# Kernel optimization log

Hardware: AMD Instinct MI355X
Metric: run time of the kernel (lower is better)

The kernel has to match this reference:

```python
import jax, jax.numpy as jnp
import numpy as np

W_SZ = 128  # window size
H = 8       # heads
DH = 64     # dim per head


def _ln(x, w, b):
    mu = x.mean(-1, keepdims=True)
    var = ((x - mu) ** 2).mean(-1, keepdims=True)
    return (x - mu) / jnp.sqrt(var + 1e-5) * w + b


def _rot_half(x):
    x1, x2 = jnp.split(x, 2, axis=-1)
    return jnp.concatenate([-x2, x1], axis=-1)


def _split_heads(t):  # [b, n, h*d] -> [b*h, n, d]
    b, n, hd = t.shape
    return t.reshape(b, n, H, hd // H).transpose(0, 2, 1, 3).reshape(b * H, n, hd // H)


def _merge_heads(t):  # [b*h, n, d] -> [b, n, h*d]
    bh, n, d = t.shape
    return t.reshape(bh // H, H, n, d).transpose(0, 2, 1, 3).reshape(bh // H, n, H * d)


def _poolformer(tokens, tok_emb, gpos_emb, g_norm_w, g_norm_b, g_Wq, g_Wkv, g_Wo, g_bo,
                gff_norm_w, gff_norm_b, gff_W1, gff_b1, gff_W2, gff_b2,
                la_norm_w, la_norm_b, la_Wq, la_Wkv, la_Wo, la_bo,
                lff_norm_w, lff_norm_b, lff_W1, lff_b1, lff_W2, lff_b2,
                out_norm_w, out_norm_b, out_W, out_b):
    b, n = tokens.shape
    nw = n // W_SZ  # n is a multiple of W_SZ, so no padding branch is taken
    x = tok_emb[tokens]                       # [b, n, D]
    D = x.shape[-1]
    g = x.reshape(b, nw, W_SZ, D).mean(axis=2) + gpos_emb[:nw][None]  # [b, nw, D]
    # inline rotary freqs over dim_head (SinusoidalEmbeddings)
    inv_freq = 1.0 / (10000.0 ** (jnp.arange(0, DH, 2, dtype=jnp.float32) / DH))
    fr = jnp.arange(n, dtype=jnp.float32)[:, None] * inv_freq[None, :]
    freqs = jnp.concatenate([fr, fr], axis=-1)  # [n, DH]
    cos_f, sin_f = jnp.cos(freqs), jnp.sin(freqs)
    scale = DH ** -0.5
    # causal masks (True = masked out)
    lmask = jnp.arange(2 * W_SZ)[None, :] > (jnp.arange(W_SZ)[:, None] + W_SZ)  # [W, 2W]
    gmask = jnp.arange(nw - 1)[None, :] >= jnp.arange(nw)[:, None]              # [nw, nw-1]
    full_mask = jnp.concatenate([
        jnp.broadcast_to(gmask[:, None, :], (nw, W_SZ, nw - 1)),
        jnp.broadcast_to(lmask[None], (nw, W_SZ, 2 * W_SZ)),
    ], axis=-1)[None]
    depth = la_Wq.shape[0]
    for l in range(depth):
        # --- global-token transformer (weights shared across layers) ---
        gn = _ln(g, g_norm_w, g_norm_b).reshape(b * nw, 1, D)
        ctx = jnp.concatenate([gn, x.reshape(b * nw, W_SZ, D)], axis=1)  # with_self=True
        q = _split_heads(gn @ g_Wq)
        k, v = jnp.split(ctx @ g_Wkv, 2, axis=-1)
        k = _split_heads(k); v = _split_heads(v)
        # causal mask is vacuous here (i=1, j=1+W -> triu diag beyond matrix)
        attn = jax.nn.softmax(jnp.einsum('bid,bjd->bij', q, k) * (k.shape[-1] ** -0.5), axis=-1)
        go = _merge_heads(jnp.einsum('bij,bjd->bid', attn, v)) @ g_Wo + g_bo
        g = g + go.reshape(b, nw, D)
        gn = _ln(g, gff_norm_w, gff_norm_b)
        g = g + (jax.nn.gelu(gn @ gff_W1 + gff_b1, approximate=False) @ gff_W2 + gff_b2)
        # --- local windowed attention with global tokens ---
        xn = _ln(x, la_norm_w[l], la_norm_b[l])
        q = _split_heads(xn @ la_Wq[l])
        k, v = jnp.split(xn @ la_Wkv[l], 2, axis=-1)
        k = _split_heads(k)
        q = q * cos_f + _rot_half(q) * sin_f
        k = k * cos_f + _rot_half(k) * sin_f
        qw = q.reshape(b * H, nw, W_SZ, DH)
        kpad = jnp.pad(k.reshape(b * H, nw, W_SZ, DH), ((0, 0), (1, 0), (0, 0), (0, 0)))
        kcat = jnp.concatenate([kpad[:, :-1], kpad[:, 1:]], axis=2)  # [bH, nw, 2W, DH]
        vcat = kcat  # faithful to source closure bug: v is overwritten with windowed k
        gk, gv = jnp.split(g[:, :-1] @ la_Wkv[l], 2, axis=-1)  # global tokens -> kv (un-normed)
        gk = _split_heads(gk); gv = _split_heads(gv)           # [bH, nw-1, DH]
        kf = jnp.concatenate([jnp.broadcast_to(gk[:, None], (b * H, nw, nw - 1, DH)), kcat], axis=2)
        vf = jnp.concatenate([jnp.broadcast_to(gv[:, None], (b * H, nw, nw - 1, DH)), vcat], axis=2)
        sim = jnp.einsum('bwid,bwjd->bwij', qw, kf) * scale
        sim = jnp.where(full_mask, -jnp.finfo(sim.dtype).max, sim)
        ao = jnp.einsum('bwij,bwjd->bwid', jax.nn.softmax(sim, axis=-1), vf)
        x = x + _merge_heads(ao.reshape(b * H, n, DH)) @ la_Wo[l] + la_bo[l]
        xn = _ln(x, lff_norm_w[l], lff_norm_b[l])
        x = x + (jax.nn.gelu(xn @ lff_W1[l] + lff_b1[l], approximate=False) @ lff_W2[l] + lff_b2[l])
    return _ln(x, out_norm_w, out_norm_b) @ out_W + out_b


def setup_inputs() -> dict:
    key = jax.random.key(0)
    ks = jax.random.split(key, 16)
    B, N, D, V, DEPTH, FF = 1, 2048, 512, 32000, 2, 2048
    INNER = H * DH
    s = 0.02
    rn = lambda k, shape: jax.random.normal(k, shape, dtype=jnp.float32) * s
    inp = {}
    inp['tokens'] = jax.random.randint(ks[0], (B, N), 0, V, dtype=jnp.int32)
    inp['tok_emb'] = rn(ks[1], (V, D))
    inp['gpos_emb'] = rn(ks[2], (N // W_SZ, D))
    inp['g_norm_w'] = jnp.ones((D,)); inp['g_norm_b'] = jnp.zeros((D,))
    inp['g_Wq'] = rn(ks[3], (D, INNER)); inp['g_Wkv'] = rn(ks[4], (D, 2 * INNER))
    inp['g_Wo'] = rn(ks[5], (INNER, D)); inp['g_bo'] = jnp.zeros((D,))
    inp['gff_norm_w'] = jnp.ones((D,)); inp['gff_norm_b'] = jnp.zeros((D,))
    inp['gff_W1'] = rn(ks[6], (D, FF)); inp['gff_b1'] = jnp.zeros((FF,))
    inp['gff_W2'] = rn(ks[7], (FF, D)); inp['gff_b2'] = jnp.zeros((D,))
    inp['la_norm_w'] = jnp.ones((DEPTH, D)); inp['la_norm_b'] = jnp.zeros((DEPTH, D))
    inp['la_Wq'] = rn(ks[8], (DEPTH, D, INNER)); inp['la_Wkv'] = rn(ks[9], (DEPTH, D, 2 * INNER))
    inp['la_Wo'] = rn(ks[10], (DEPTH, INNER, D)); inp['la_bo'] = jnp.zeros((DEPTH, D))
    inp['lff_norm_w'] = jnp.ones((DEPTH, D)); inp['lff_norm_b'] = jnp.zeros((DEPTH, D))
    inp['lff_W1'] = rn(ks[11], (DEPTH, D, FF)); inp['lff_b1'] = jnp.zeros((DEPTH, FF))
    inp['lff_W2'] = rn(ks[12], (DEPTH, FF, D)); inp['lff_b2'] = jnp.zeros((DEPTH, D))
    inp['out_norm_w'] = jnp.ones((D,)); inp['out_norm_b'] = jnp.zeros((D,))
    inp['out_W'] = rn(ks[13], (D, V)); inp['out_b'] = jnp.zeros((V,))
    return inp


def reference(tokens, tok_emb, gpos_emb, g_norm_w, g_norm_b, g_Wq, g_Wkv, g_Wo, g_bo,
              gff_norm_w, gff_norm_b, gff_W1, gff_b1, gff_W2, gff_b2,
              la_norm_w, la_norm_b, la_Wq, la_Wkv, la_Wo, la_bo,
              lff_norm_w, lff_norm_b, lff_W1, lff_b1, lff_W2, lff_b2,
              out_norm_w, out_norm_b, out_W, out_b):
    return _poolformer(tokens, tok_emb, gpos_emb, g_norm_w, g_norm_b, g_Wq, g_Wkv, g_Wo, g_bo,
                       gff_norm_w, gff_norm_b, gff_W1, gff_b1, gff_W2, gff_b2,
                       la_norm_w, la_norm_b, la_Wq, la_Wkv, la_Wo, la_bo,
                       lff_norm_w, lff_norm_b, lff_W1, lff_b1, lff_W2, lff_b2,
                       out_norm_w, out_norm_b, out_W, out_b)
```

## Files before the change

kernel.cpp:

```cpp
#include <hip/hip_runtime.h>
#include <math.h>

#define N_TOK 2048
#define DM    512
#define NW    16
#define WSZ   128
#define NH    8
#define DHD   64
#define FFD   2048
#define VOC   32000
#define NDEPTH 2

typedef unsigned short u16;
typedef unsigned int   u32;
typedef __attribute__((ext_vector_type(8))) short bf16x8;
typedef __attribute__((ext_vector_type(4))) float f32x4;

__device__ __forceinline__ float gelu_f(float v){
  return 0.5f*v*(1.0f+erff(v*0.70710678118654752440f));
}
__device__ __forceinline__ u16 f2bf(float f){
  u32 u = __float_as_uint(f);
  u += 0x7fffu + ((u >> 16) & 1u);
  return (u16)(u >> 16);
}

__global__ void k_embed(const int* __restrict__ tok, const float* __restrict__ emb,
                        float* __restrict__ x, u16* __restrict__ xb){
  int idx = blockIdx.x*256 + threadIdx.x;
  int i = idx >> 9, d = idx & 511;
  float v = emb[(size_t)tok[i]*DM + d];
  x[idx] = v;
  xb[idx] = f2bf(v);
}

__global__ void k_pool(const float* __restrict__ x, const float* __restrict__ gpos,
                       float* __restrict__ g){
  int idx = blockIdx.x*256 + threadIdx.x;
  int w = idx >> 9, d = idx & 511;
  const float* p = x + (size_t)(w*WSZ)*DM + d;
  float s = 0.f;
  #pragma unroll 8
  for (int i=0;i<WSZ;i++) s += p[(size_t)i*DM];
  g[idx] = s*(1.f/WSZ) + gpos[idx];
}

__global__ void k_rotab(float* __restrict__ ct, float* __restrict__ st){
  int idx = blockIdx.x*256 + threadIdx.x;
  int i = idx >> 5, j = idx & 31;
  double inv = pow(10000.0, -(double)j/32.0);
  double a = (double)i*inv;
  ct[idx] = (float)cos(a);
  st[idx] = (float)sin(a);
}

__global__ void k_rope(float* __restrict__ q, float* __restrict__ k,
                       const float* __restrict__ ct, const float* __restrict__ st){
  int idx = blockIdx.x*256 + threadIdx.x;
  int i = idx >> 8;
  int h = (idx >> 5) & 7;
  int j = idx & 31;
  float c = ct[i*32+j], s = st[i*32+j];
  size_t base = (size_t)i*DM + h*DHD + j;
  float q0=q[base], q1=q[base+32];
  q[base]    = q0*c - q1*s;
  q[base+32] = q1*c + q0*s;
  float k0=k[base], k1=k[base+32];
  k[base]    = k0*c - k1*s;
  k[base+32] = k1*c + k0*s;
}

template<bool BF>
__global__ __launch_bounds__(256) void k_ln(const float* __restrict__ in,
                     float* __restrict__ outf, u16* __restrict__ outb,
                     const float* __restrict__ w, const float* __restrict__ b){
  int r = blockIdx.x;
  const float2* p2 = reinterpret_cast<const float2*>(in + (size_t)r*DM);
  float2 v = p2[threadIdx.x];
  float s = v.x+v.y, ss = v.x*v.x + v.y*v.y;
  #pragma unroll
  for (int o=32;o;o>>=1){ s += __shfl_xor(s,o); ss += __shfl_xor(ss,o); }
  __shared__ float sm[4], sm2[4];
  int wv = threadIdx.x >> 6;
  if ((threadIdx.x & 63) == 0){ sm[wv]=s; sm2[wv]=ss; }
  __syncthreads();
  if (threadIdx.x == 0){
    float t=sm[0]+sm[1]+sm[2]+sm[3], t2=sm2[0]+sm2[1]+sm2[2]+sm2[3];
    float mu = t*(1.f/DM);
    float var = t2*(1.f/DM) - mu*mu;
    sm[0]=mu; sm2[0]=rsqrtf(var + 1e-5f);
  }
  __syncthreads();
  float mu = sm[0], rs = sm2[0];
  float2 wv2 = reinterpret_cast<const float2*>(w)[threadIdx.x];
  float2 bv2 = reinterpret_cast<const float2*>(b)[threadIdx.x];
  float ox = (v.x-mu)*rs*wv2.x + bv2.x;
  float oy = (v.y-mu)*rs*wv2.y + bv2.y;
  if (BF){
    reinterpret_cast<u32*>(outb)[(size_t)r*256 + threadIdx.x] =
        (u32)f2bf(ox) | ((u32)f2bf(oy) << 16);
  } else {
    float2 o; o.x = ox; o.y = oy;
    reinterpret_cast<float2*>(outf + (size_t)r*DM)[threadIdx.x] = o;
  }
}

__global__ __launch_bounds__(256) void k_wcvt(const float* __restrict__ in, int ldn, int c0,
                        u16* __restrict__ out, int K){
  __shared__ float t[32][33];
  const int tx = threadIdx.x & 31, ty = threadIdx.x >> 5;
  const int n0 = blockIdx.x*32, k0 = blockIdx.y*32;
  #pragma unroll
  for (int r = ty; r < 32; r += 8)
    t[r][tx] = in[(size_t)(k0+r)*ldn + c0 + n0 + tx];
  __syncthreads();
  #pragma unroll
  for (int r = ty; r < 32; r += 8)
    out[(size_t)(n0+r)*K + k0 + tx] = f2bf(t[tx][r]);
}

template<bool BIAS,bool RES,bool GELU,bool SBF,bool SF32>
__global__ __launch_bounds__(256) void k_mgemm(
    const u16* __restrict__ A, int lda,
    const u16* __restrict__ Bt,
    float* __restrict__ C, int ldc,
    u16* __restrict__ Cb, int ldcb,
    const float* __restrict__ bias, int K)
{
  __shared__ __align__(16) u16 As[128*40];
  __shared__ __align__(16) u16 Bs[128*40];
  const int tid = threadIdx.x;
  const int bm0 = blockIdx.y*128, bn0 = blockIdx.x*128;
  const int lane = tid & 63, wid = tid >> 6;
  const int wr = wid >> 1, wc = wid & 1;
  const int r16 = lane & 15, ko = lane >> 4;
  const int srow = tid >> 1, koff = (tid & 1) * 16;
  const u16* Ap = A + (size_t)(bm0 + srow)*lda + koff;
  const u16* Bp = Bt + (size_t)(bn0 + srow)*K + koff;
  const u32 lwa = (u32)srow*40 + (u32)koff;

  f32x4 acc[4][4];
  #pragma unroll
  for (int m=0;m<4;m++)
    #pragma unroll
    for (int n=0;n<4;n++)
      acc[m][n] = (f32x4){0.f,0.f,0.f,0.f};

  for (int kk = 0; kk < K; kk += 32){
    const uint4 a0 = *reinterpret_cast<const uint4*>(Ap + kk);
    const uint4 a1 = *reinterpret_cast<const uint4*>(Ap + kk + 8);
    const uint4 b0 = *reinterpret_cast<const uint4*>(Bp + kk);
    const uint4 b1 = *reinterpret_cast<const uint4*>(Bp + kk + 8);
    *reinterpret_cast<uint4*>(&As[lwa])     = a0;
    *reinterpret_cast<uint4*>(&As[lwa + 8]) = a1;
    *reinterpret_cast<uint4*>(&Bs[lwa])     = b0;
    *reinterpret_cast<uint4*>(&Bs[lwa + 8]) = b1;
    __syncthreads();
    bf16x8 af[4], bfr[4];
    #pragma unroll
    for (int m=0;m<4;m++)
      af[m] = *reinterpret_cast<const bf16x8*>(&As[(u32)(wr*64 + m*16 + r16)*40 + (u32)ko*8]);
    #pragma unroll
    for (int n=0;n<4;n++)
      bfr[n] = *reinterpret_cast<const bf16x8*>(&Bs[(u32)(wc*64 + n*16 + r16)*40 + (u32)ko*8]);
    #pragma unroll
    for (int m=0;m<4;m++)
      #pragma unroll
      for (int n=0;n<4;n++)
        acc[m][n] = __builtin_amdgcn_mfma_f32_16x16x32_bf16(af[m], bfr[n], acc[m][n], 0, 0, 0);
    __syncthreads();
  }

  const int crow0 = bm0 + wr*64, ccol0 = bn0 + wc*64;
  #pragma unroll
  for (int m=0;m<4;m++){
    #pragma unroll
    for (int j=0;j<4;j++){
      const int row = crow0 + m*16 + ko*4 + j;
      #pragma unroll
      for (int n=0;n<4;n++){
        const int col = ccol0 + n*16 + r16;
        float v = acc[m][n][j];
        if (BIAS) v += bias[col];
        if (GELU) v = gelu_f(v);
        if (RES)  v += C[(size_t)row*ldc + col];
        if (SF32) C[(size_t)row*ldc + col] = v;
        if (SBF)  Cb[(size_t)row*ldcb + col] = f2bf(v);
      }
    }
  }
}

__global__ __launch_bounds__(256) void k_psum(
    const float* __restrict__ A, int lda,
    const float* __restrict__ B, int ldb,
    float* __restrict__ P, int N, int M)
{
  __shared__ __align__(16) float As[16][68];
  const int tid = threadIdx.x;
  const int cg = tid & 63, rg = tid >> 6;
  const int n0 = blockIdx.x*256 + cg*4;
  const int k0 = blockIdx.y*64;
  for (int e = tid; e < 16*64; e += 256){
    int r = e >> 6, c = e & 63;
    As[r][c] = (r < M) ? A[(size_t)r*lda + k0 + c] : 0.f;
  }
  __syncthreads();
  float4 acc0 = {0.f,0.f,0.f,0.f}, acc1 = acc0, acc2 = acc0, acc3 = acc0;
  const float* Bp = B + (size_t)k0*ldb + n0;
  #pragma unroll 4
  for (int k4 = 0; k4 < 64; k4 += 4){
    float a0[4], a1[4], a2[4], a3[4];
    *reinterpret_cast<float4*>(a0) = *reinterpret_cast<const float4*>(&As[rg*4+0][k4]);
    *reinterpret_cast<float4*>(a1) = *reinterpret_cast<const float4*>(&As[rg*4+1][k4]);
    *reinterpret_cast<float4*>(a2) = *reinterpret_cast<const float4*>(&As[rg*4+2][k4]);
    *reinterpret_cast<float4*>(a3) = *reinterpret_cast<const float4*>(&As[rg*4+3][k4]);
    #pragma unroll
    for (int j = 0; j < 4; j++){
      const float4 bv = *reinterpret_cast<const float4*>(Bp + (size_t)(k4+j)*ldb);
      acc0.x = fmaf(a0[j], bv.x, acc0.x); acc0.y = fmaf(a0[j], bv.y, acc0.y);
      acc0.z = fmaf(a0[j], bv.z, acc0.z); acc0.w = fmaf(a0[j], bv.w, acc0.w);
      acc1.x = fmaf(a1[j], bv.x, acc1.x); acc1.y = fmaf(a1[j], bv.y, acc1.y);
      acc1.z = fmaf(a1[j], bv.z, acc1.z); acc1.w = fmaf(a1[j], bv.w, acc1.w);
      acc2.x = fmaf(a2[j], bv.x, acc2.x); acc2.y = fmaf(a2[j], bv.y, acc2.y);
      acc2.z = fmaf(a2[j], bv.z, acc2.z); acc2.w = fmaf(a2[j], bv.w, acc2.w);
      acc3.x = fmaf(a3[j], bv.x, acc3.x); acc3.y = fmaf(a3[j], bv.y, acc3.y);
      acc3.z = fmaf(a3[j], bv.z, acc3.z); acc3.w = fmaf(a3[j], bv.w, acc3.w);
    }
  }
  float* Pp = P + ((size_t)blockIdx.y*16 + rg*4)*N + n0;
  *reinterpret_cast<float4*>(Pp)       = acc0;
  *reinterpret_cast<float4*>(Pp + N)   = acc1;
  *reinterpret_cast<float4*>(Pp + 2*N) = acc2;
  *reinterpret_cast<float4*>(Pp + 3*N) = acc3;
}

template<bool BIAS,bool RES,bool GELU>
__global__ __launch_bounds__(256) void k_red(
    const float* __restrict__ P, int N, int S, int M,
    float* __restrict__ C, int ldc, const float* __restrict__ bias)
{
  int idx = blockIdx.x*256 + threadIdx.x;
  int r = idx / N, n = idx - r*N;
  if (r >= M) return;
  float v = 0.f;
  for (int s = 0; s < S; s++) v += P[((size_t)s*16 + r)*N + n];
  if (BIAS) v += bias[n];
  if (GELU) v = gelu_f(v);
  if (RES)  v += C[(size_t)r*ldc + n];
  C[(size_t)r*ldc + n] = v;
}

__global__ __launch_bounds__(64) void k_gattn(
    const float* __restrict__ gq, const float* __restrict__ kvg,
    const float* __restrict__ kvx, float* __restrict__ out)
{
  const int w = blockIdx.x >> 3, h = blockIdx.x & 7;
  const int lane = threadIdx.x;
  __shared__ float qs[64];
  __shared__ float p[129];
  qs[lane] = gq[(size_t)w*DM + h*DHD + lane];
  __syncthreads();
  for (int c=0;c<3;c++){
    int j = c*64 + lane;
    if (j < 129){
      const float* kp = (j==0) ? &kvg[(size_t)w*1024 + h*DHD]
                               : &kvx[(size_t)(w*WSZ + j-1)*1024 + h*DHD];
      float s = 0.f;
      for (int d=0;d<64;d++) s = fmaf(qs[d], kp[d], s);
      p[j] = s*0.125f;
    }
  }
  __syncthreads();
  float mx = -3.4e38f;
  for (int j=lane;j<129;j+=64) mx = fmaxf(mx, p[j]);
  #pragma unroll
  for (int o=32;o;o>>=1) mx = fmaxf(mx, __shfl_xor(mx,o));
  float sum = 0.f;
  for (int j=lane;j<129;j+=64){ float e = expf(p[j]-mx); p[j]=e; sum+=e; }
  #pragma unroll
  for (int o=32;o;o>>=1) sum += __shfl_xor(sum,o);
  const float rs = 1.f/sum;
  __syncthreads();
  float o_ = 0.f;
  for (int j=0;j<129;j++){
    const float* vp = (j==0) ? &kvg[(size_t)w*1024 + 512 + h*DHD]
                             : &kvx[(size_t)(w*WSZ + j-1)*1024 + 512 + h*DHD];
    o_ = fmaf(p[j], vp[lane], o_);
  }
  out[(size_t)w*DM + h*DHD + lane] = o_*rs;
}

__global__ __launch_bounds__(256) void k_lattn_m(
    const float* __restrict__ q, const float* __restrict__ k,
    const float* __restrict__ gkv, u16* __restrict__ ob)
{
  __shared__ __align__(16) u16 smem[43136];
  __shared__ float rsum[64];
  u16* Ks = smem;
  u16* Qs = smem + 19584;
  u16* Vt = smem + 24192;
  u16* Ps = smem;
  const int bid = blockIdx.x;
  const int half = bid & 1, h = (bid >> 1) & 7, w = bid >> 4;
  const int tid = threadIdx.x;
  const int lane = tid & 63, wv = tid >> 6;
  const int c16 = lane & 15, ko = lane >> 4;
  const int q0 = w*WSZ + half*64;
  #pragma unroll
  for (int t = 0; t < 16; t++){
    int e = tid + t*256, r = e >> 6, c = e & 63;
    Qs[(u32)r*72 + c] = f2bf(q[(size_t)(q0 + r)*DM + h*DHD + c]);
  }
  #pragma unroll
  for (int t = 0; t < 68; t++){
    int e = tid + t*256, r = e >> 6, c = e & 63;
    float v;
    if (r < 15) v = gkv[(size_t)r*1024 + h*DHD + c];
    else if (r < 271){
      int m = r - 15;
      if (m < 128) v = (w == 0) ? 0.f : k[(size_t)((w-1)*WSZ + m)*DM + h*DHD + c];
      else         v = k[(size_t)(w*WSZ + (m-128))*DM + h*DHD + c];
    } else v = 0.f;
    Ks[(u32)r*72 + c] = f2bf(v);
  }
  __syncthreads();
  #pragma unroll
  for (int t = 0; t < 72; t++){
    int e = tid + t*256, j = e >> 6, c = e & 63;
    u16 v;
    if (j < 15)       v = f2bf(gkv[(size_t)j*1024 + 512 + h*DHD + c]);
    else if (j < 272) v = Ks[(u32)j*72 + c];
    else              v = 0;
    Vt[(u32)c*296 + j] = v;
  }
  f32x4 acc[17];
  {
    const bf16x8 aq0 = *reinterpret_cast<const bf16x8*>(&Qs[(u32)(wv*16 + c16)*72 + ko*8]);
    const bf16x8 aq1 = *reinterpret_cast<const bf16x8*>(&Qs[(u32)(wv*16 + c16)*72 + ko*8 + 32]);
    #pragma unroll
    for (int n = 0; n < 17; n++){
      const bf16x8 b0 = *reinterpret_cast<const bf16x8*>(&Ks[(u32)(n*16 + c16)*72 + ko*8]);
      const bf16x8 b1 = *reinterpret_cast<const bf16x8*>(&Ks[(u32)(n*16 + c16)*72 + ko*8 + 32]);
      f32x4 a_ = (f32x4){0.f,0.f,0.f,0.f};
      a_ = __builtin_amdgcn_mfma_f32_16x16x32_bf16(aq0, b0, a_, 0, 0, 0);
      a_ = __builtin_amdgcn_mfma_f32_16x16x32_bf16(aq1, b1, a_, 0, 0, 0);
      acc[n] = a_;
    }
  }
  __syncthreads();
  float mx[4] = {-3.4e38f,-3.4e38f,-3.4e38f,-3.4e38f};
  #pragma unroll
  for (int n = 0; n < 17; n++){
    const int jkey = n*16 + c16;
    #pragma unroll
    for (int jr = 0; jr < 4; jr++){
      const int qi = half*64 + wv*16 + ko*4 + jr;
      bool vis;
      if (jkey < 15)        vis = (jkey < w);
      else if (jkey < 271)  vis = ((jkey - 15) <= qi + 128);
      else                  vis = false;
      float s = vis ? acc[n][jr]*0.125f : -3.4e38f;
      acc[n][jr] = s;
      mx[jr] = fmaxf(mx[jr], s);
    }
  }
  #pragma unroll
  for (int o = 1; o < 16; o <<= 1)
    #pragma unroll
    for (int jr = 0; jr < 4; jr++) mx[jr] = fmaxf(mx[jr], __shfl_xor(mx[jr], o));
  float sum[4] = {0.f,0.f,0.f,0.f};
  #pragma unroll
  for (int n = 0; n < 17; n++)
    #pragma unroll
    for (int jr = 0; jr < 4; jr++){
      float p = expf(acc[n][jr] - mx[jr]);
      sum[jr] += p;
      Ps[(u32)(wv*16 + ko*4 + jr)*296 + n*16 + c16] = f2bf(p);
    }
  #pragma unroll
  for (int o = 1; o < 16; o <<= 1)
    #pragma unroll
    for (int jr = 0; jr < 4; jr++) sum[jr] += __shfl_xor(sum[jr], o);
  if (c16 == 0){
    #pragma unroll
    for (int jr = 0; jr < 4; jr++) rsum[wv*16 + ko*4 + jr] = sum[jr];
  }
  #pragma unroll
  for (int z = 0; z < 4; z++){
    int e = lane + z*64;
    Ps[(u32)(wv*16 + (e >> 4))*296 + 272 + (e & 15)] = 0;
  }
  f32x4 o_[4];
  #pragma unroll
  for (int n = 0; n < 4; n++) o_[n] = (f32x4){0.f,0.f,0.f,0.f};
  #pragma unroll
  for (int ks = 0; ks < 9; ks++){
    const bf16x8 ap = *reinterpret_cast<const bf16x8*>(&Ps[(u32)(wv*16 + c16)*296 + ko*8 + ks*32]);
    #pragma unroll
    for (int n = 0; n < 4; n++){
      const bf16x8 bv = *reinterpret_cast<const bf16x8*>(&Vt[(u32)(n*16 + c16)*296 + ko*8 + ks*32]);
      o_[n] = __builtin_amdgcn_mfma_f32_16x16x32_bf16(ap, bv, o_[n], 0, 0, 0);
    }
  }
  #pragma unroll
  for (int jr = 0; jr < 4; jr++){
    const int r = wv*16 + ko*4 + jr;
    const float rs = 1.f / rsum[r];
    #pragma unroll
    for (int n = 0; n < 4; n++)
      ob[(size_t)(q0 + r)*DM + h*DHD + n*16 + c16] = f2bf(o_[n][jr] * rs);
  }
}

extern "C" void kernel_launch(void* const* d_in, const int* in_sizes, int n_in,
                              void* d_out, int out_size, void* d_ws, size_t ws_size,
                              hipStream_t stream)
{
  (void)in_sizes; (void)n_in; (void)out_size; (void)ws_size;
  const int*   tokens   = (const int*)  d_in[0];
  const float* tok_emb  = (const float*)d_in[1];
  const float* gpos_emb = (const float*)d_in[2];
  const float* g_norm_w = (const float*)d_in[3];
  const float* g_norm_b = (const float*)d_in[4];
  const float* g_Wq     = (const float*)d_in[5];
  const float* g_Wkv    = (const float*)d_in[6];
  const float* g_Wo     = (const float*)d_in[7];
  const float* g_bo     = (const float*)d_in[8];
  const float* gffnw    = (const float*)d_in[9];
  const float* gffnb    = (const float*)d_in[10];
  const float* gff_W1   = (const float*)d_in[11];
  const float* gff_b1   = (const float*)d_in[12];
  const float* gff_W2   = (const float*)d_in[13];
  const float* gff_b2   = (const float*)d_in[14];
  const float* la_nw    = (const float*)d_in[15];
  const float* la_nb    = (const float*)d_in[16];
  const float* la_Wq    = (const float*)d_in[17];
  const float* la_Wkv   = (const float*)d_in[18];
  const float* la_Wo    = (const float*)d_in[19];
  const float* la_bo    = (const float*)d_in[20];
  const float* lff_nw   = (const float*)d_in[21];
  const float* lff_nb   = (const float*)d_in[22];
  const float* lff_W1   = (const float*)d_in[23];
  const float* lff_b1   = (const float*)d_in[24];
  const float* lff_W2   = (const float*)d_in[25];
  const float* lff_b2   = (const float*)d_in[26];
  const float* out_nw   = (const float*)d_in[27];
  const float* out_nb   = (const float*)d_in[28];
  const float* out_W    = (const float*)d_in[29];
  const float* out_b    = (const float*)d_in[30];
  float* O = (float*)d_out;

  float* ws = (float*)d_ws;
  float* x    = ws;
  float* qb   = x + 1048576;
  float* kb   = qb + 1048576;
  float* g    = kb + 1048576;
  float* gn   = g + 8192;
  float* gq   = gn + 8192;
  float* gao  = gq + 8192;
  float* gkvg = gao + 8192;
  float* gh1  = gkvg + 16384;
  float* gkvl = gh1 + 32768;
  float* ct   = gkvl + 15360;
  float* st   = ct + 65536;
  u16* xb     = (u16*)(st + 65536);
  u16* xnb    = xb + 1048576;
  u16* aob    = xnb + 1048576;
  u16* h1b    = aob + 1048576;
  u16* Wt_voc = h1b + 4194304;
  u16* Wt_gkv = Wt_voc + 16384000;
  u16* Wt_ff1 = Wt_gkv + 524288;
  u16* Wt_ff2 = Wt_ff1 + 2097152;
  u16* Wt_q   = Wt_ff2 + 2097152;
  u16* Wt_k   = Wt_q + 524288;
  u16* Wt_o   = Wt_k + 524288;
  float* P    = (float*)h1b;

  k_wcvt<<<dim3(VOC/32, 16), 256, 0, stream>>>(out_W, VOC, 0, Wt_voc, DM);
  k_wcvt<<<dim3(32, 16),     256, 0, stream>>>(g_Wkv, 1024, 0, Wt_gkv, DM);
  for (int l=0;l<NDEPTH;l++){
    k_wcvt<<<dim3(64, 16), 256, 0, stream>>>(lff_W1 + (size_t)l*DM*FFD, FFD, 0, Wt_ff1 + (size_t)l*1048576, DM);
    k_wcvt<<<dim3(16, 64), 256, 0, stream>>>(lff_W2 + (size_t)l*FFD*DM, DM, 0, Wt_ff2 + (size_t)l*1048576, FFD);
    k_wcvt<<<dim3(16, 16), 256, 0, stream>>>(la_Wq  + (size_t)l*DM*DM, DM, 0, Wt_q + (size_t)l*262144, DM);
    k_wcvt<<<dim3(16, 16), 256, 0, stream>>>(la_Wkv + (size_t)l*DM*1024, 1024, 0, Wt_k + (size_t)l*262144, DM);
    k_wcvt<<<dim3(16, 16), 256, 0, stream>>>(la_Wo  + (size_t)l*DM*DM, DM, 0, Wt_o + (size_t)l*262144, DM);
  }

  k_embed<<<N_TOK*DM/256, 256, 0, stream>>>(tokens, tok_emb, x, xb);
  k_pool <<<NW*DM/256,   256, 0, stream>>>(x, gpos_emb, g);
  k_rotab<<<N_TOK*32/256,256, 0, stream>>>(ct, st);

  for (int l=0;l<NDEPTH;l++){
    k_ln<false><<<NW,256,0,stream>>>(g, gn, nullptr, g_norm_w, g_norm_b);
    k_psum<<<dim3(4,8),256,0,stream>>>(gn, DM, g_Wkv, 1024, P, 1024, NW);
    k_red<false,false,false><<<64,256,0,stream>>>(P, 1024, 8, NW, gkvg, 1024, nullptr);
    k_psum<<<dim3(2,8),256,0,stream>>>(gn, DM, g_Wq, 512, P, 512, NW);
    k_red<false,false,false><<<32,256,0,stream>>>(P, 512, 8, NW, gq, 512, nullptr);
    k_mgemm<false,false,false,false,true><<<dim3(8,16),256,0,stream>>>(xb, DM, Wt_gkv, qb, 1024, nullptr, 0, nullptr, DM);
    k_gattn<<<NW*NH,64,0,stream>>>(gq, gkvg, qb, gao);
    k_psum<<<dim3(2,8),256,0,stream>>>(gao, DM, g_Wo, DM, P, 512, NW);
    k_red<true,true,false><<<32,256,0,stream>>>(P, 512, 8, NW, g, DM, g_bo);
    k_ln<false><<<NW,256,0,stream>>>(g, gn, nullptr, gffnw, gffnb);
    k_psum<<<dim3(8,8),256,0,stream>>>(gn, DM, gff_W1, FFD, P, FFD, NW);
    k_red<true,false,true><<<128,256,0,stream>>>(P, FFD, 8, NW, gh1, FFD, gff_b1);
    k_psum<<<dim3(2,32),256,0,stream>>>(gh1, FFD, gff_W2, DM, P, 512, NW);
    k_red<true,true,false><<<32,256,0,stream>>>(P, 512, 32, NW, g, DM, gff_b2);
    k_psum<<<dim3(4,8),256,0,stream>>>(g, DM, la_Wkv + (size_t)l*DM*1024, 1024, P, 1024, 15);
    k_red<false,false,false><<<64,256,0,stream>>>(P, 1024, 8, 15, gkvl, 1024, nullptr);
    k_ln<true><<<N_TOK,256,0,stream>>>(x, nullptr, xnb, la_nw + l*DM, la_nb + l*DM);
    k_mgemm<false,false,false,false,true><<<dim3(4,16),256,0,stream>>>(xnb, DM, Wt_q + (size_t)l*262144, qb, DM, nullptr, 0, nullptr, DM);
    k_mgemm<false,false,false,false,true><<<dim3(4,16),256,0,stream>>>(xnb, DM, Wt_k + (size_t)l*262144, kb, DM, nullptr, 0, nullptr, DM);
    k_rope<<<N_TOK*NH*32/256,256,0,stream>>>(qb, kb, ct, st);
    k_lattn_m<<<NW*NH*2,256,0,stream>>>(qb, kb, gkvl, aob);
    k_mgemm<true,true,false,true,true><<<dim3(4,16),256,0,stream>>>(aob, DM, Wt_o + (size_t)l*262144, x, DM, xb, DM, la_bo + l*DM, DM);
    k_ln<true><<<N_TOK,256,0,stream>>>(x, nullptr, xnb, lff_nw + l*DM, lff_nb + l*DM);
    k_mgemm<true,false,true,true,false><<<dim3(16,16),256,0,stream>>>(xnb, DM, Wt_ff1 + (size_t)l*1048576, nullptr, 0, h1b, FFD, lff_b1 + l*FFD, DM);
    k_mgemm<true,true,false,true,true><<<dim3(4,16),256,0,stream>>>(h1b, FFD, Wt_ff2 + (size_t)l*1048576, x, DM, xb, DM, lff_b2 + l*DM, FFD);
  }
  k_ln<true><<<N_TOK,256,0,stream>>>(x, nullptr, xnb, out_nw, out_nb);
  k_mgemm<true,false,false,false,true><<<dim3(VOC/128,16),256,0,stream>>>(xnb, DM, Wt_voc, O, VOC, nullptr, 0, out_b, DM);
}
```

Measured before the change: 1.277 ms.

## Use direct global-to-LDS loads with swizzled tiles and templated GEMM tile sizes

The bf16 MFMA GEMM now uses global_load_lds to copy 16-byte chunks straight into shared memory. Tiles are XOR-swizzled and K-steps are 64 wide, which cuts register staging and bank conflicts. Tile sizes become template parameters, so the small N=512 GEMMs launch 64x64 tiles and more blocks, improving occupancy across CUs. The global attention kernel also stages K and V in shared memory instead of doing strided global reads per dot product. The risks are fewer MFMAs per load on small tiles and direct-LDS load semantics that depend on lane layout.

```diff
diff --git a/kernel.cpp b/kernel.cpp
--- a/kernel.cpp
+++ b/kernel.cpp
@@ -23,6 +23,11 @@
   u32 u = __float_as_uint(f);
   u += 0x7fffu + ((u >> 16) & 1u);
   return (u16)(u >> 16);
+}
+__device__ __forceinline__ void gld16(const u16* g, u16* l){
+  __builtin_amdgcn_global_load_lds(
+      (const __attribute__((address_space(1))) u32*)g,
+      (__attribute__((address_space(3))) u32*)l, 16, 0, 0);
 }
 
 __global__ void k_embed(const int* __restrict__ tok, const float* __restrict__ emb,
@@ -119,7 +124,7 @@
     out[(size_t)(n0+r)*K + k0 + tx] = f2bf(t[tx][r]);
 }
 
-template<bool BIAS,bool RES,bool GELU,bool SBF,bool SF32>
+template<int BM,int BN,bool BIAS,bool RES,bool GELU,bool SBF,bool SF32>
 __global__ __launch_bounds__(256) void k_mgemm(
     const u16* __restrict__ A, int lda,
     const u16* __restrict__ Bt,
@@ -127,58 +132,71 @@
     u16* __restrict__ Cb, int ldcb,
     const float* __restrict__ bias, int K)
 {
-  __shared__ __align__(16) u16 As[128*40];
-  __shared__ __align__(16) u16 Bs[128*40];
+  constexpr int WM = BM/2, WN = BN/2;
+  constexpr int MF = WM/16, NF = WN/16;
+  constexpr int AL = BM/32, BL = BN/32;
+  __shared__ __align__(128) u16 As[BM*64];
+  __shared__ __align__(128) u16 Bs[BN*64];
   const int tid = threadIdx.x;
-  const int bm0 = blockIdx.y*128, bn0 = blockIdx.x*128;
+  const int bm0 = blockIdx.y*BM, bn0 = blockIdx.x*BN;
   const int lane = tid & 63, wid = tid >> 6;
   const int wr = wid >> 1, wc = wid & 1;
   const int r16 = lane & 15, ko = lane >> 4;
-  const int srow = tid >> 1, koff = (tid & 1) * 16;
-  const u16* Ap = A + (size_t)(bm0 + srow)*lda + koff;
-  const u16* Bp = Bt + (size_t)(bn0 + srow)*K + koff;
-  const u32 lwa = (u32)srow*40 + (u32)koff;
-
-  f32x4 acc[4][4];
-  #pragma unroll
-  for (int m=0;m<4;m++)
-    #pragma unroll
-    for (int n=0;n<4;n++)
+  const int lr8 = lane >> 3, lc8 = lane & 7;
+
+  f32x4 acc[MF][NF];
+  #pragma unroll
+  for (int m=0;m<MF;m++)
+    #pragma unroll
+    for (int n=0;n<NF;n++)
       acc[m][n] = (f32x4){0.f,0.f,0.f,0.f};
 
-  for (int kk = 0; kk < K; kk += 32){
-    const uint4 a0 = *reinterpret_cast<const uint4*>(Ap + kk);
-    const uint4 a1 = *reinterpret_cast<const uint4*>(Ap + kk + 8);
-    const uint4 b0 = *reinterpret_cast<const uint4*>(Bp + kk);
-    const uint4 b1 = *reinterpret_cast<const uint4*>(Bp + kk + 8);
-    *reinterpret_cast<uint4*>(&As[lwa])     = a0;
-    *reinterpret_cast<uint4*>(&As[lwa + 8]) = a1;
-    *reinterpret_cast<uint4*>(&Bs[lwa])     = b0;
-    *reinterpret_cast<uint4*>(&Bs[lwa + 8]) = b1;
+  for (int kk = 0; kk < K; kk += 64){
+    #pragma unroll
+    for (int t=0;t<AL;t++){
+      const int R = wid*(BM/4) + t*8;
+      const int rl = R + lr8;
+      const int ch = lc8 ^ (rl & 7);
+      gld16(A + (size_t)(bm0 + rl)*lda + kk + ch*8, &As[(u32)R*64]);
+    }
+    #pragma unroll
+    for (int t=0;t<BL;t++){
+      const int R = wid*(BN/4) + t*8;
+      const int rl = R + lr8;
+      const int ch = lc8 ^ (rl & 7);
+      gld16(Bt + (size_t)(bn0 + rl)*K + kk + ch*8, &Bs[(u32)R*64]);
+    }
     __syncthreads();
-    bf16x8 af[4], bfr[4];
-    #pragma unroll
-    for (int m=0;m<4;m++)
-      af[m] = *reinterpret_cast<const bf16x8*>(&As[(u32)(wr*64 + m*16 + r16)*40 + (u32)ko*8]);
-    #pragma unroll
-    for (int n=0;n<4;n++)
-      bfr[n] = *reinterpret_cast<const bf16x8*>(&Bs[(u32)(wc*64 + n*16 + r16)*40 + (u32)ko*8]);
-    #pragma unroll
-    for (int m=0;m<4;m++)
+    #pragma unroll
+    for (int h=0;h<2;h++){
+      bf16x8 af[MF], bfr[NF];
       #pragma unroll
-      for (int n=0;n<4;n++)
-        acc[m][n] = __builtin_amdgcn_mfma_f32_16x16x32_bf16(af[m], bfr[n], acc[m][n], 0, 0, 0);
+      for (int m=0;m<MF;m++){
+        const int ra = wr*WM + m*16 + r16;
+        af[m] = *reinterpret_cast<const bf16x8*>(&As[(u32)ra*64 + (u32)(((ko + 4*h) ^ (ra & 7))*8)]);
+      }
+      #pragma unroll
+      for (int n=0;n<NF;n++){
+        const int rb = wc*WN + n*16 + r16;
+        bfr[n] = *reinterpret_cast<const bf16x8*>(&Bs[(u32)rb*64 + (u32)(((ko + 4*h) ^ (rb & 7))*8)]);
+      }
+      #pragma unroll
+      for (int m=0;m<MF;m++)
+        #pragma unroll
+        for (int n=0;n<NF;n++)
+          acc[m][n] = __builtin_amdgcn_mfma_f32_16x16x32_bf16(af[m], bfr[n], acc[m][n], 0, 0, 0);
+    }
     __syncthreads();
   }
 
-  const int crow0 = bm0 + wr*64, ccol0 = bn0 + wc*64;
-  #pragma unroll
-  for (int m=0;m<4;m++){
+  const int crow0 = bm0 + wr*WM, ccol0 = bn0 + wc*WN;
+  #pragma unroll
+  for (int m=0;m<MF;m++){
     #pragma unroll
     for (int j=0;j<4;j++){
       const int row = crow0 + m*16 + ko*4 + j;
       #pragma unroll
-      for (int n=0;n<4;n++){
+      for (int n=0;n<NF;n++){
         const int col = ccol0 + n*16 + r16;
         float v = acc[m][n][j];
         if (BIAS) v += bias[col];
@@ -259,15 +277,20 @@
   const int lane = threadIdx.x;
   __shared__ float qs[64];
   __shared__ float p[129];
+  __shared__ float KV[129][65];
   qs[lane] = gq[(size_t)w*DM + h*DHD + lane];
+  for (int e = lane; e < 129*64; e += 64){
+    int j = e >> 6, d = e & 63;
+    KV[j][d] = (j==0) ? kvg[(size_t)w*1024 + h*DHD + d]
+                      : kvx[(size_t)(w*WSZ + j-1)*1024 + h*DHD + d];
+  }
   __syncthreads();
   for (int c=0;c<3;c++){
     int j = c*64 + lane;
     if (j < 129){
-      const float* kp = (j==0) ? &kvg[(size_t)w*1024 + h*DHD]
-                               : &kvx[(size_t)(w*WSZ + j-1)*1024 + h*DHD];
       float s = 0.f;
-      for (int d=0;d<64;d++) s = fmaf(qs[d], kp[d], s);
+      #pragma unroll
+      for (int d=0;d<64;d++) s = fmaf(qs[d], KV[j][d], s);
       p[j] = s*0.125f;
     }
   }
@@ -282,12 +305,15 @@
   for (int o=32;o;o>>=1) sum += __shfl_xor(sum,o);
   const float rs = 1.f/sum;
   __syncthreads();
+  for (int e = lane; e < 129*64; e += 64){
+    int j = e >> 6, d = e & 63;
+    KV[j][d] = (j==0) ? kvg[(size_t)w*1024 + 512 + h*DHD + d]
+                      : kvx[(size_t)(w*WSZ + j-1)*1024 + 512 + h*DHD + d];
+  }
+  __syncthreads();
   float o_ = 0.f;
-  for (int j=0;j<129;j++){
-    const float* vp = (j==0) ? &kvg[(size_t)w*1024 + 512 + h*DHD]
-                             : &kvx[(size_t)(w*WSZ + j-1)*1024 + 512 + h*DHD];
-    o_ = fmaf(p[j], vp[lane], o_);
-  }
+  #pragma unroll 8
+  for (int j=0;j<129;j++) o_ = fmaf(p[j], KV[j][lane], o_);
   out[(size_t)w*DM + h*DHD + lane] = o_*rs;
 }
 
@@ -497,7 +523,7 @@
     k_red<false,false,false><<<64,256,0,stream>>>(P, 1024, 8, NW, gkvg, 1024, nullptr);
     k_psum<<<dim3(2,8),256,0,stream>>>(gn, DM, g_Wq, 512, P, 512, NW);
     k_red<false,false,false><<<32,256,0,stream>>>(P, 512, 8, NW, gq, 512, nullptr);
-    k_mgemm<false,false,false,false,true><<<dim3(8,16),256,0,stream>>>(xb, DM, Wt_gkv, qb, 1024, nullptr, 0, nullptr, DM);
+    k_mgemm<64,128,false,false,false,false,true><<<dim3(8,32),256,0,stream>>>(xb, DM, Wt_gkv, qb, 1024, nullptr, 0, nullptr, DM);
     k_gattn<<<NW*NH,64,0,stream>>>(gq, gkvg, qb, gao);
     k_psum<<<dim3(2,8),256,0,stream>>>(gao, DM, g_Wo, DM, P, 512, NW);
     k_red<true,true,false><<<32,256,0,stream>>>(P, 512, 8, NW, g, DM, g_bo);
@@ -509,15 +535,15 @@
     k_psum<<<dim3(4,8),256,0,stream>>>(g, DM, la_Wkv + (size_t)l*DM*1024, 1024, P, 1024, 15);
     k_red<false,false,false><<<64,256,0,stream>>>(P, 1024, 8, 15, gkvl, 1024, nullptr);
     k_ln<true><<<N_TOK,256,0,stream>>>(x, nullptr, xnb, la_nw + l*DM, la_nb + l*DM);
-    k_mgemm<false,false,false,false,true><<<dim3(4,16),256,0,stream>>>(xnb, DM, Wt_q + (size_t)l*262144, qb, DM, nullptr, 0, nullptr, DM);
-    k_mgemm<false,false,false,false,true><<<dim3(4,16),256,0,stream>>>(xnb, DM, Wt_k + (size_t)l*262144, kb, DM, nullptr, 0, nullptr, DM);
+    k_mgemm<64,64,false,false,false,false,true><<<dim3(8,32),256,0,stream>>>(xnb, DM, Wt_q + (size_t)l*262144, qb, DM, nullptr, 0, nullptr, DM);
+    k_mgemm<64,64,false,false,false,false,true><<<dim3(8,32),256,0,stream>>>(xnb, DM, Wt_k + (size_t)l*262144, kb, DM, nullptr, 0, nullptr, DM);
     k_rope<<<N_TOK*NH*32/256,256,0,stream>>>(qb, kb, ct, st);
     k_lattn_m<<<NW*NH*2,256,0,stream>>>(qb, kb, gkvl, aob);
-    k_mgemm<true,true,false,true,true><<<dim3(4,16),256,0,stream>>>(aob, DM, Wt_o + (size_t)l*262144, x, DM, xb, DM, la_bo + l*DM, DM);
+    k_mgemm<64,64,true,true,false,true,true><<<dim3(8,32),256,0,stream>>>(aob, DM, Wt_o + (size_t)l*262144, x, DM, xb, DM, la_bo + l*DM, DM);
     k_ln<true><<<N_TOK,256,0,stream>>>(x, nullptr, xnb, lff_nw + l*DM, lff_nb + l*DM);
-    k_mgemm<true,false,true,true,false><<<dim3(16,16),256,0,stream>>>(xnb, DM, Wt_ff1 + (size_t)l*1048576, nullptr, 0, h1b, FFD, lff_b1 + l*FFD, DM);
-    k_mgemm<true,true,false,true,true><<<dim3(4,16),256,0,stream>>>(h1b, FFD, Wt_ff2 + (size_t)l*1048576, x, DM, xb, DM, lff_b2 + l*DM, FFD);
+    k_mgemm<128,128,true,false,true,true,false><<<dim3(16,16),256,0,stream>>>(xnb, DM, Wt_ff1 + (size_t)l*1048576, nullptr, 0, h1b, FFD, lff_b1 + l*FFD, DM);
+    k_mgemm<64,64,true,true,false,true,true><<<dim3(8,32),256,0,stream>>>(h1b, FFD, Wt_ff2 + (size_t)l*1048576, x, DM, xb, DM, lff_b2 + l*DM, FFD);
   }
   k_ln<true><<<N_TOK,256,0,stream>>>(x, nullptr, xnb, out_nw, out_nb);
-  k_mgemm<true,false,false,false,true><<<dim3(VOC/128,16),256,0,stream>>>(xnb, DM, Wt_voc, O, VOC, nullptr, 0, out_b, DM);
-}
+  k_mgemm<128,128,true,false,false,false,true><<<dim3(VOC/128,16),256,0,stream>>>(xnb, DM, Wt_voc, O, VOC, nullptr, 0, out_b, DM);
+}
```

New measurement: 1.153 ms. -9.7%, faster.
